# Kernel optimization log

Hardware: AMD Instinct MI355X
Metric: run time of the kernel (lower is better)

Reference implementation:

```python
import jax, jax.numpy as jnp
import numpy as np

B, S, E, H = 4, 2048, 1024, 16
HD = E // H


def setup_inputs() -> dict:
    key = jax.random.key(0)
    ks = jax.random.split(key, 7)
    scale = 1.0 / np.sqrt(E)
    return {
        "query": jax.random.normal(ks[0], (B, S, E), dtype=jnp.float32),
        "key": jax.random.normal(ks[1], (B, S, E), dtype=jnp.float32),
        "value": jax.random.normal(ks[2], (B, S, E), dtype=jnp.float32),
        "Wqkv": jax.random.normal(ks[3], (3 * E, E), dtype=jnp.float32) * scale,
        "bqkv": jnp.zeros((3 * E,), dtype=jnp.float32),
        "Wout": jax.random.normal(ks[4], (E, E), dtype=jnp.float32) * scale,
        "bout": jnp.zeros((E,), dtype=jnp.float32),
    }


def reference(query, key, value, Wqkv, bqkv, Wout, bout):
    # key/value are ignored by the original module (QKV all from query).
    b, s, e = query.shape
    qkv = query @ Wqkv.T + bqkv                       # [B,S,3E]
    qkv = qkv.reshape(b, s, 3, H, HD)
    q = jnp.transpose(qkv[:, :, 0], (0, 2, 1, 3))     # [B,H,S,HD]
    k = jnp.transpose(qkv[:, :, 1], (0, 2, 1, 3))
    v = jnp.transpose(qkv[:, :, 2], (0, 2, 1, 3))
    # NOTE: original scales by embed_dim**0.5, not head_dim**0.5
    scores = jnp.einsum("bhqd,bhkd->bhqk", q, k) / jnp.sqrt(jnp.float32(e))
    attn = jax.nn.softmax(scores, axis=-1)            # dropout = identity (eval)
    out = jnp.einsum("bhqk,bhkd->bhqd", attn, v)      # [B,H,S,HD]
    out = jnp.transpose(out, (0, 2, 1, 3)).reshape(b, s, e)
    return out @ Wout.T + bout
```

## Files before the change

### kernel.cpp

```cpp
#include <hip/hip_runtime.h>
#include <stdint.h>


typedef __bf16 bf16;
typedef __bf16 bf16x8 __attribute__((ext_vector_type(8)));
typedef __bf16 bf16x4 __attribute__((ext_vector_type(4)));
typedef float  f32x4  __attribute__((ext_vector_type(4)));
typedef float  f32x16 __attribute__((ext_vector_type(16)));
typedef unsigned u32x4 __attribute__((ext_vector_type(4)));

#define MFMA16(a, b, c) __builtin_amdgcn_mfma_f32_16x16x32_bf16((a), (b), (c), 0, 0, 0)
#define MFMA32(a, b, c) __builtin_amdgcn_mfma_f32_32x32x16_bf16((a), (b), (c), 0, 0, 0)

__device__ __forceinline__ void gload16(const void* g, void* l) {
  __builtin_amdgcn_global_load_lds(
      (const __attribute__((address_space(1))) void*)g,
      (__attribute__((address_space(3))) void*)l, 16, 0, 0);
}

__device__ __forceinline__ uint32_t lds_off(const void* p) {
  return (uint32_t)(uintptr_t)(__attribute__((address_space(3))) const void*)p;
}

__device__ __forceinline__ bf16x4 tr16(uint32_t off) {
  bf16x4 d;
  asm volatile("ds_read_b64_tr_b16 %0, %1" : "=&v"(d) : "v"(off));
  return d;
}

__global__ __launch_bounds__(256) void cvt_all(const float* __restrict__ a,
                                               const float* __restrict__ b,
                                               const float* __restrict__ c,
                                               bf16* __restrict__ out,
                                               int na4, int nb4, int nc4) {
  const int i = blockIdx.x * 256 + threadIdx.x;
  const float4* src;
  int j = i;
  if (i < na4) {
    src = (const float4*)a;
  } else if (i < na4 + nb4) {
    src = (const float4*)b; j = i - na4;
  } else if (i < na4 + nb4 + nc4) {
    src = (const float4*)c; j = i - na4 - nb4;
  } else {
    return;
  }
  const float4 v = src[j];
  bf16x4 o;
  o[0] = (bf16)v.x; o[1] = (bf16)v.y; o[2] = (bf16)v.z; o[3] = (bf16)v.w;
  ((bf16x4*)out)[i] = o;
}

template <typename OutT>
__global__ __launch_bounds__(256, 2) void gemm_bt(const bf16* __restrict__ A,
                                                  const bf16* __restrict__ Bt,
                                                  const float* __restrict__ bias,
                                                  OutT* __restrict__ C,
                                                  int M, int N, int K,
                                                  int sc_lo, int sc_hi, float scv) {
  __shared__ bf16 As[128 * 32];
  __shared__ bf16 Bs[128 * 32];
  const int tid = threadIdx.x;
  const int lane = tid & 63, wid = tid >> 6;
  const int l15 = lane & 15, lg = lane >> 4;
  const int wr = wid >> 1, wc = wid & 1;
  const int row0 = blockIdx.y * 128, col0 = blockIdx.x * 128;
  const float cscale = (col0 >= sc_lo && col0 < sc_hi) ? scv : 1.0f;

  f32x4 acc[4][4];
#pragma unroll
  for (int m = 0; m < 4; ++m)
#pragma unroll
    for (int n = 0; n < 4; ++n) acc[m][n] = (f32x4){0.f, 0.f, 0.f, 0.f};

  for (int k0 = 0; k0 < K; k0 += 32) {
    __syncthreads();
#pragma unroll
    for (int j = 0; j < 2; ++j) {
      const int c = j * 256 + tid;
      const int r = c >> 2, cb = (c & 3) << 4;
      gload16((const char*)(A + (size_t)(row0 + r) * K + k0) + cb, (char*)As + c * 16);
      gload16((const char*)(Bt + (size_t)(col0 + r) * K + k0) + cb, (char*)Bs + c * 16);
    }
    __syncthreads();

    bf16x8 af[4], bfr[4];
#pragma unroll
    for (int m = 0; m < 4; ++m)
      af[m] = *(const bf16x8*)(As + ((wr * 64 + m * 16 + l15) << 5) + lg * 8);
#pragma unroll
    for (int n = 0; n < 4; ++n)
      bfr[n] = *(const bf16x8*)(Bs + ((wc * 64 + n * 16 + l15) << 5) + lg * 8);
#pragma unroll
    for (int m = 0; m < 4; ++m)
#pragma unroll
      for (int n = 0; n < 4; ++n) acc[m][n] = MFMA16(af[m], bfr[n], acc[m][n]);
  }

#pragma unroll
  for (int m = 0; m < 4; ++m) {
    const int grow0 = row0 + wr * 64 + m * 16 + lg * 4;
#pragma unroll
    for (int n = 0; n < 4; ++n) {
      const int gcol = col0 + wc * 64 + n * 16 + l15;
      const float bv = bias[gcol];
#pragma unroll
      for (int i = 0; i < 4; ++i)
        C[(size_t)(grow0 + i) * N + gcol] = (OutT)((acc[m][n][i] + bv) * cscale);
    }
  }
}

__global__ __launch_bounds__(256, 4) void attn_fwd(const bf16* __restrict__ qkv,
                                                   bf16* __restrict__ aout) {
  __shared__ bf16 Ks[2][64 * 64];
  __shared__ bf16 Vs[2][64 * 64];
  __shared__ float bc[4][32];

  const int bid = blockIdx.x;
  const int xcd = bid & 7, slot = bid >> 3;
  const int g = xcd + 8 * (slot >> 4);
  const int qblk = slot & 15;
  const int h = g & 15, b = g >> 4;

  const int tid = threadIdx.x, wid = tid >> 6, lane = tid & 63;
  const int l31 = lane & 31, hh = lane >> 5, l15 = lane & 15;
  const int b4 = (lane >> 4) & 1;
  const bf16* qbase = qkv + (size_t)b * 2048 * 3072;

  bf16x8 qf[4];
  {
    const bf16* qp = qbase + (size_t)(qblk * 128 + wid * 32 + l31) * 3072 + h * 64 + hh * 8;
    qf[0] = *(const bf16x8*)(qp);
    qf[1] = *(const bf16x8*)(qp + 16);
    qf[2] = *(const bf16x8*)(qp + 32);
    qf[3] = *(const bf16x8*)(qp + 48);
  }

  const char* ksrc[2]; const char* vsrc[2];
  int kdo[2], vdo[2];
#pragma unroll
  for (int j = 0; j < 2; ++j) {
    const int c = j * 256 + tid;
    {
      const int key = c >> 3;
      const int db = (((c & 7) ^ (key & 7)) << 4);
      ksrc[j] = (const char*)(qbase + (size_t)key * 3072 + 1024 + h * 64) + db;
      kdo[j] = c * 16;
    }
    {
      const int s = c >> 3, jj = c & 7;
      const int vkey = ((s >> 2) << 2) + (jj >> 1);
      const int vd = ((s & 3) << 4) + ((jj & 1) << 3);
      vsrc[j] = (const char*)(qbase + (size_t)vkey * 3072 + 2048 + h * 64 + vd);
      vdo[j] = c * 16;
    }
  }
  const size_t tadv = (size_t)64 * 3072 * 2;

  f32x16 o0, o1;
#pragma unroll
  for (int i = 0; i < 16; ++i) { o0[i] = 0.f; o1[i] = 0.f; }
  float lrow = 0.f;

  const uint32_t vsb0 = lds_off(&Vs[0][0]) + (uint32_t)(l15 * 8);

  gload16(ksrc[0], (char*)&Ks[0][0] + kdo[0]);
  gload16(ksrc[1], (char*)&Ks[0][0] + kdo[1]);
  gload16(vsrc[0], (char*)&Vs[0][0] + vdo[0]);
  gload16(vsrc[1], (char*)&Vs[0][0] + vdo[1]);

  for (int kt = 0; kt < 32; ++kt) {
    const int cur = kt & 1;
    if (kt < 31) {
      const size_t off = (size_t)(kt + 1) * tadv;
      char* kb = (char*)&Ks[cur ^ 1][0];
      char* vb = (char*)&Vs[cur ^ 1][0];
      gload16(ksrc[0] + off, kb + kdo[0]);
      gload16(ksrc[1] + off, kb + kdo[1]);
      gload16(vsrc[0] + off, vb + vdo[0]);
      gload16(vsrc[1] + off, vb + vdo[1]);
      __builtin_amdgcn_sched_barrier(0);
      asm volatile("s_waitcnt vmcnt(4)" ::: "memory");
    } else {
      __builtin_amdgcn_sched_barrier(0);
      asm volatile("s_waitcnt vmcnt(0)" ::: "memory");
    }
    __builtin_amdgcn_s_barrier();
    __builtin_amdgcn_sched_barrier(0);

    const char* ksb = (const char*)&Ks[cur][0];
    const uint32_t vbb = vsb0 + (uint32_t)(cur * 8192);

    f32x16 st0, st1;
#pragma unroll
    for (int i = 0; i < 16; ++i) { st0[i] = 0.f; st1[i] = 0.f; }
    __builtin_amdgcn_s_setprio(1);
#pragma unroll
    for (int k2 = 0; k2 < 4; ++k2) {
      const int dby = k2 * 32 + hh * 16;
      bf16x8 kf0 = *(const bf16x8*)(ksb + ((l31 * 128 + dby) ^ ((l31 & 7) << 4)));
      st0 = MFMA32(kf0, qf[k2], st0);
      bf16x8 kf1 = *(const bf16x8*)(ksb + (((l31 + 32) * 128 + dby) ^ ((l31 & 7) << 4)));
      st1 = MFMA32(kf1, qf[k2], st1);
    }
    __builtin_amdgcn_s_setprio(0);

    float ps0 = 0.f, ps1 = 0.f;
#pragma unroll
    for (int i = 0; i < 16; ++i) {
      st0[i] = __builtin_amdgcn_exp2f(st0[i]);
      st1[i] = __builtin_amdgcn_exp2f(st1[i]);
      ps0 += st0[i];
      ps1 += st1[i];
    }
    float ps = ps0 + ps1;
    ps += __shfl_xor(ps, 32);
    lrow += ps;

    uint32_t w[16];
#pragma unroll
    for (int j = 0; j < 8; ++j) {
      asm("v_cvt_pk_bf16_f32 %0, %1, %2" : "=v"(w[j]) : "v"(st0[2 * j]), "v"(st0[2 * j + 1]));
      asm("v_cvt_pk_bf16_f32 %0, %1, %2" : "=v"(w[8 + j]) : "v"(st1[2 * j]), "v"(st1[2 * j + 1]));
    }
#pragma unroll
    for (int g2 = 0; g2 < 4; ++g2) {
      asm volatile("v_permlane32_swap_b32 %0, %1" : "+v"(w[4 * g2]), "+v"(w[4 * g2 + 2]));
      asm volatile("v_permlane32_swap_b32 %0, %1" : "+v"(w[4 * g2 + 1]), "+v"(w[4 * g2 + 3]));
    }
    bf16x8 pf[4];
#pragma unroll
    for (int k2 = 0; k2 < 4; ++k2) {
      u32x4 t;
      t[0] = w[4 * k2]; t[1] = w[4 * k2 + 1]; t[2] = w[4 * k2 + 2]; t[3] = w[4 * k2 + 3];
      pf[k2] = __builtin_bit_cast(bf16x8, t);
    }

#pragma unroll
    for (int db = 0; db < 2; ++db) {
      bf16x4 va[4], vb2[4];
#pragma unroll
      for (int k2 = 0; k2 < 4; ++k2) {
        const uint32_t s0 = (uint32_t)((((k2 * 4 + hh * 2) * 4) + db * 2 + b4) * 128);
        va[k2]  = tr16(vbb + s0);
        vb2[k2] = tr16(vbb + s0 + 512);
      }
      asm volatile("s_waitcnt lgkmcnt(0)" ::: "memory");
      __builtin_amdgcn_sched_barrier(0);
      __builtin_amdgcn_s_setprio(1);
#pragma unroll
      for (int k2 = 0; k2 < 4; ++k2) {
        bf16x8 vf;
#pragma unroll
        for (int e = 0; e < 4; ++e) { vf[e] = va[k2][e]; vf[e + 4] = vb2[k2][e]; }
        if (db == 0) o0 = MFMA32(pf[k2], vf, o0);
        else         o1 = MFMA32(pf[k2], vf, o1);
      }
      __builtin_amdgcn_s_setprio(0);
    }
    __builtin_amdgcn_sched_barrier(0);
    __builtin_amdgcn_s_barrier();
  }

  if (lane < 32) bc[wid][l31] = 1.0f / lrow;
  bf16* ob = aout + ((size_t)b * 2048 + qblk * 128 + wid * 32) * 1024 + h * 64;
#pragma unroll
  for (int r = 0; r < 16; ++r) {
    const int row = (r & 3) + 8 * (r >> 2) + 4 * hh;
    const float inv = bc[wid][row];
    ob[(size_t)row * 1024 + l31]      = (bf16)(o0[r] * inv);
    ob[(size_t)row * 1024 + 32 + l31] = (bf16)(o1[r] * inv);
  }
}

extern "C" void kernel_launch(void* const* d_in, const int* in_sizes, int n_in,
                              void* d_out, int out_size, void* d_ws, size_t ws_size,
                              hipStream_t stream) {
  const float* query = (const float*)d_in[0];
  const float* Wqkv = (const float*)d_in[3];
  const float* bqkv = (const float*)d_in[4];
  const float* Wout = (const float*)d_in[5];
  const float* bout = (const float*)d_in[6];
  float* out = (float*)d_out;

  constexpr int M = 8192;
  constexpr int E = 1024, E3 = 3072;
  constexpr float SC = 0.045084220f;

  bf16* q_bf    = (bf16*)d_ws;
  bf16* wqkv_bf = q_bf + (size_t)M * E;
  bf16* wout_bf = wqkv_bf + (size_t)E3 * E;
  bf16* qkv_bf  = wout_bf + (size_t)E * E;
  bf16* aout_bf = qkv_bf + (size_t)M * E3;

  constexpr int na4 = M * E / 4, nb4 = E3 * E / 4, nc4 = E * E / 4;
  cvt_all<<<(na4 + nb4 + nc4 + 255) / 256, 256, 0, stream>>>(
      query, Wqkv, Wout, q_bf, na4, nb4, nc4);

  gemm_bt<bf16><<<dim3(E3 / 128, M / 128), 256, 0, stream>>>(
      q_bf, wqkv_bf, bqkv, qkv_bf, M, E3, E, E, 2 * E, SC);
  attn_fwd<<<1024, 256, 0, stream>>>(qkv_bf, aout_bf);
  gemm_bt<float><<<dim3(E / 128, M / 128), 256, 0, stream>>>(
      aout_bf, wout_bf, bout, out, M, E, E, 0, 0, 1.0f);
}
```

Measured before the change: 192.2 us.

## Double attention query tile to 256 rows with 512-thread blocks sharing K/V tiles

After: 196.8 us. 2.4% more time.

```diff
diff --git a/kernel.cpp b/kernel.cpp
--- a/kernel.cpp
+++ b/kernel.cpp
@@ -7,6 +7,7 @@
 typedef __bf16 bf16x4 __attribute__((ext_vector_type(4)));
 typedef float  f32x4  __attribute__((ext_vector_type(4)));
 typedef float  f32x16 __attribute__((ext_vector_type(16)));
+typedef unsigned u32x2 __attribute__((ext_vector_type(2)));
 typedef unsigned u32x4 __attribute__((ext_vector_type(4)));
 
 #define MFMA16(a, b, c) __builtin_amdgcn_mfma_f32_16x16x32_bf16((a), (b), (c), 0, 0, 0)
@@ -26,6 +27,20 @@
   bf16x4 d;
   asm volatile("ds_read_b64_tr_b16 %0, %1" : "=&v"(d) : "v"(off));
   return d;
+}
+template <int IMM>
+__device__ __forceinline__ bf16x4 tr16o(uint32_t off) {
+  bf16x4 d;
+  asm volatile("ds_read_b64_tr_b16 %0, %1 offset:%2" : "=&v"(d) : "v"(off), "i"(IMM));
+  return d;
+}
+
+__device__ __forceinline__ bf16x8 vpack(bf16x4 lo, bf16x4 hi) {
+  const u32x2 a = __builtin_bit_cast(u32x2, lo);
+  const u32x2 b = __builtin_bit_cast(u32x2, hi);
+  u32x4 t;
+  t[0] = a[0]; t[1] = a[1]; t[2] = b[0]; t[3] = b[1];
+  return __builtin_bit_cast(bf16x8, t);
 }
 
 __global__ __launch_bounds__(256) void cvt_all(const float* __restrict__ a,
@@ -111,16 +126,16 @@
   }
 }
 
-__global__ __launch_bounds__(256, 4) void attn_fwd(const bf16* __restrict__ qkv,
+__global__ __launch_bounds__(512, 4) void attn_fwd(const bf16* __restrict__ qkv,
                                                    bf16* __restrict__ aout) {
   __shared__ bf16 Ks[2][64 * 64];
   __shared__ bf16 Vs[2][64 * 64];
-  __shared__ float bc[4][32];
+  __shared__ float bc[8][32];
 
   const int bid = blockIdx.x;
   const int xcd = bid & 7, slot = bid >> 3;
-  const int g = xcd + 8 * (slot >> 4);
-  const int qblk = slot & 15;
+  const int g = xcd + 8 * (slot >> 3);
+  const int qblk = slot & 7;
   const int h = g & 15, b = g >> 4;
 
   const int tid = threadIdx.x, wid = tid >> 6, lane = tid & 63;
@@ -130,30 +145,29 @@
 
   bf16x8 qf[4];
   {
-    const bf16* qp = qbase + (size_t)(qblk * 128 + wid * 32 + l31) * 3072 + h * 64 + hh * 8;
+    const bf16* qp = qbase + (size_t)(qblk * 256 + wid * 32 + l31) * 3072 + h * 64 + hh * 8;
     qf[0] = *(const bf16x8*)(qp);
     qf[1] = *(const bf16x8*)(qp + 16);
     qf[2] = *(const bf16x8*)(qp + 32);
     qf[3] = *(const bf16x8*)(qp + 48);
   }
 
-  const char* ksrc[2]; const char* vsrc[2];
-  int kdo[2], vdo[2];
-#pragma unroll
-  for (int j = 0; j < 2; ++j) {
-    const int c = j * 256 + tid;
+  const char* ksrc; const char* vsrc;
+  int kdo, vdo;
+  {
+    const int c = tid;
     {
       const int key = c >> 3;
       const int db = (((c & 7) ^ (key & 7)) << 4);
-      ksrc[j] = (const char*)(qbase + (size_t)key * 3072 + 1024 + h * 64) + db;
-      kdo[j] = c * 16;
+      ksrc = (const char*)(qbase + (size_t)key * 3072 + 1024 + h * 64) + db;
+      kdo = c * 16;
     }
     {
       const int s = c >> 3, jj = c & 7;
       const int vkey = ((s >> 2) << 2) + (jj >> 1);
       const int vd = ((s & 3) << 4) + ((jj & 1) << 3);
-      vsrc[j] = (const char*)(qbase + (size_t)vkey * 3072 + 2048 + h * 64 + vd);
-      vdo[j] = c * 16;
+      vsrc = (const char*)(qbase + (size_t)vkey * 3072 + 2048 + h * 64 + vd);
+      vdo = c * 16;
     }
   }
   const size_t tadv = (size_t)64 * 3072 * 2;
@@ -163,25 +177,19 @@
   for (int i = 0; i < 16; ++i) { o0[i] = 0.f; o1[i] = 0.f; }
   float lrow = 0.f;
 
-  const uint32_t vsb0 = lds_off(&Vs[0][0]) + (uint32_t)(l15 * 8);
-
-  gload16(ksrc[0], (char*)&Ks[0][0] + kdo[0]);
-  gload16(ksrc[1], (char*)&Ks[0][0] + kdo[1]);
-  gload16(vsrc[0], (char*)&Vs[0][0] + vdo[0]);
-  gload16(vsrc[1], (char*)&Vs[0][0] + vdo[1]);
+  const uint32_t vbase = lds_off(&Vs[0][0]) + (uint32_t)(l15 * 8 + hh * 1024 + b4 * 128);
+
+  gload16(ksrc, (char*)&Ks[0][0] + kdo);
+  gload16(vsrc, (char*)&Vs[0][0] + vdo);
 
   for (int kt = 0; kt < 32; ++kt) {
     const int cur = kt & 1;
     if (kt < 31) {
       const size_t off = (size_t)(kt + 1) * tadv;
-      char* kb = (char*)&Ks[cur ^ 1][0];
-      char* vb = (char*)&Vs[cur ^ 1][0];
-      gload16(ksrc[0] + off, kb + kdo[0]);
-      gload16(ksrc[1] + off, kb + kdo[1]);
-      gload16(vsrc[0] + off, vb + vdo[0]);
-      gload16(vsrc[1] + off, vb + vdo[1]);
+      gload16(ksrc + off, (char*)&Ks[cur ^ 1][0] + kdo);
+      gload16(vsrc + off, (char*)&Vs[cur ^ 1][0] + vdo);
       __builtin_amdgcn_sched_barrier(0);
-      asm volatile("s_waitcnt vmcnt(4)" ::: "memory");
+      asm volatile("s_waitcnt vmcnt(2)" ::: "memory");
     } else {
       __builtin_amdgcn_sched_barrier(0);
       asm volatile("s_waitcnt vmcnt(0)" ::: "memory");
@@ -190,7 +198,7 @@
     __builtin_amdgcn_sched_barrier(0);
 
     const char* ksb = (const char*)&Ks[cur][0];
-    const uint32_t vbb = vsb0 + (uint32_t)(cur * 8192);
+    const uint32_t vb_cur = vbase + (uint32_t)(cur * 8192);
 
     f32x16 st0, st1;
 #pragma unroll
@@ -237,26 +245,37 @@
       pf[k2] = __builtin_bit_cast(bf16x8, t);
     }
 
-#pragma unroll
-    for (int db = 0; db < 2; ++db) {
+    {
       bf16x4 va[4], vb2[4];
-#pragma unroll
-      for (int k2 = 0; k2 < 4; ++k2) {
-        const uint32_t s0 = (uint32_t)((((k2 * 4 + hh * 2) * 4) + db * 2 + b4) * 128);
-        va[k2]  = tr16(vbb + s0);
-        vb2[k2] = tr16(vbb + s0 + 512);
-      }
+      va[0] = tr16o<0 * 2048 + 0>(vb_cur);
+      vb2[0] = tr16o<0 * 2048 + 512>(vb_cur);
+      va[1] = tr16o<1 * 2048 + 0>(vb_cur);
+      vb2[1] = tr16o<1 * 2048 + 512>(vb_cur);
+      va[2] = tr16o<2 * 2048 + 0>(vb_cur);
+      vb2[2] = tr16o<2 * 2048 + 512>(vb_cur);
+      va[3] = tr16o<3 * 2048 + 0>(vb_cur);
+      vb2[3] = tr16o<3 * 2048 + 512>(vb_cur);
       asm volatile("s_waitcnt lgkmcnt(0)" ::: "memory");
       __builtin_amdgcn_sched_barrier(0);
       __builtin_amdgcn_s_setprio(1);
 #pragma unroll
-      for (int k2 = 0; k2 < 4; ++k2) {
-        bf16x8 vf;
-#pragma unroll
-        for (int e = 0; e < 4; ++e) { vf[e] = va[k2][e]; vf[e + 4] = vb2[k2][e]; }
-        if (db == 0) o0 = MFMA32(pf[k2], vf, o0);
-        else         o1 = MFMA32(pf[k2], vf, o1);
-      }
+      for (int k2 = 0; k2 < 4; ++k2)
+        o0 = MFMA32(pf[k2], vpack(va[k2], vb2[k2]), o0);
+      __builtin_amdgcn_s_setprio(0);
+      va[0] = tr16o<0 * 2048 + 256 + 0>(vb_cur);
+      vb2[0] = tr16o<0 * 2048 + 256 + 512>(vb_cur);
+      va[1] = tr16o<1 * 2048 + 256 + 0>(vb_cur);
+      vb2[1] = tr16o<1 * 2048 + 256 + 512>(vb_cur);
+      va[2] = tr16o<2 * 2048 + 256 + 0>(vb_cur);
+      vb2[2] = tr16o<2 * 2048 + 256 + 512>(vb_cur);
+      va[3] = tr16o<3 * 2048 + 256 + 0>(vb_cur);
+      vb2[3] = tr16o<3 * 2048 + 256 + 512>(vb_cur);
+      asm volatile("s_waitcnt lgkmcnt(0)" ::: "memory");
+      __builtin_amdgcn_sched_barrier(0);
+      __builtin_amdgcn_s_setprio(1);
+#pragma unroll
+      for (int k2 = 0; k2 < 4; ++k2)
+        o1 = MFMA32(pf[k2], vpack(va[k2], vb2[k2]), o1);
       __builtin_amdgcn_s_setprio(0);
     }
     __builtin_amdgcn_sched_barrier(0);
@@ -264,7 +283,7 @@
   }
 
   if (lane < 32) bc[wid][l31] = 1.0f / lrow;
-  bf16* ob = aout + ((size_t)b * 2048 + qblk * 128 + wid * 32) * 1024 + h * 64;
+  bf16* ob = aout + ((size_t)b * 2048 + qblk * 256 + wid * 32) * 1024 + h * 64;
 #pragma unroll
   for (int r = 0; r < 16; ++r) {
     const int row = (r & 3) + 8 * (r >> 2) + 4 * hh;
@@ -300,7 +319,7 @@
 
   gemm_bt<bf16><<<dim3(E3 / 128, M / 128), 256, 0, stream>>>(
       q_bf, wqkv_bf, bqkv, qkv_bf, M, E3, E, E, 2 * E, SC);
-  attn_fwd<<<1024, 256, 0, stream>>>(qkv_bf, aout_bf);
+  attn_fwd<<<512, 512, 0, stream>>>(qkv_bf, aout_bf);
   gemm_bt<float><<<dim3(E / 128, M / 128), 256, 0, stream>>>(
       aout_bf, wout_bf, bout, out, M, E, E, 0, 0, 1.0f);
 }
```
